# Kernel optimization log

Measured on AMD Instinct MI355X. Metric: run time of the kernel, lower is better.

Reference implementation:

```python
import jax, jax.numpy as jnp
import numpy as np


def setup_inputs() -> dict:
    key = jax.random.key(0)
    ks = jax.random.split(key, 5)
    B, H, W, C = 4, 64, 64, 256
    d = C // 8
    x = jax.random.normal(ks[0], (B, H, W, C), dtype=jnp.float32)
    Wq = jax.random.normal(ks[1], (C, d), dtype=jnp.float32) * (1.0 / np.sqrt(C))
    bq = jnp.zeros((d,), dtype=jnp.float32)
    Wk = jax.random.normal(ks[2], (C, d), dtype=jnp.float32) * (1.0 / np.sqrt(C))
    bk = jnp.zeros((d,), dtype=jnp.float32)
    Wv = jax.random.normal(ks[3], (C, C), dtype=jnp.float32) * (1.0 / np.sqrt(C))
    bv = jnp.zeros((C,), dtype=jnp.float32)
    gamma = jnp.zeros((), dtype=jnp.float32)
    return {"x": x, "Wq": Wq, "bq": bq, "Wk": Wk, "bk": bk, "Wv": Wv, "bv": bv, "gamma": gamma}


def reference(x, Wq, bq, Wk, bk, Wv, bv, gamma):
    B, H, W, C = x.shape
    N = H * W
    xt = x.reshape(B, N, C)  # 1x1 conv == per-pixel dense
    q = xt @ Wq + bq                        # [B, N, d]
    k = xt @ Wk + bk                        # [B, N, d]
    v = xt @ Wv + bv                        # [B, N, C]
    energy = jnp.einsum('bnd,bmd->bnm', q, k)   # Q K^T, [B, N, N]
    attn = jax.nn.softmax(energy, axis=-1)
    # tf: out = matmul(V^T[B,C,N], attn)[B,C,N] then transpose -> out[b,j,c] = sum_i v[b,i,c]*attn[b,i,j]
    out = jnp.einsum('bic,bij->bjc', v, attn)   # [B, N, C]
    out = out.reshape(B, H, W, C)
    return gamma * out + x
```

## Files before the change

kernel.cpp:

```cpp
#include <hip/hip_runtime.h>
#include <hip/hip_bf16.h>


typedef __attribute__((ext_vector_type(4)))  float    f32x4;
typedef __attribute__((ext_vector_type(16))) float    f32x16;
typedef __attribute__((ext_vector_type(8)))  short    bf8;
typedef __attribute__((ext_vector_type(4)))  short    bf4;
typedef __attribute__((ext_vector_type(4)))  unsigned u32x4;

__device__ __forceinline__ short f2bf(float f) {
    unsigned u = __builtin_bit_cast(unsigned, f);
    u += 0x7FFF + ((u >> 16) & 1);
    return (short)(u >> 16);
}
__device__ __forceinline__ float bf2f(short h) {
    unsigned u = ((unsigned)(unsigned short)h) << 16;
    return __builtin_bit_cast(float, u);
}
__device__ __forceinline__ unsigned cvtpk(float lo, float hi) {
    unsigned r;
    asm("v_cvt_pk_bf16_f32 %0, %1, %2" : "=v"(r) : "v"(lo), "v"(hi));
    return r;
}
__device__ __forceinline__ float exp2_fast(float x) {
    float r;
    asm("v_exp_f32 %0, %1" : "=v"(r) : "v"(x));
    return r;
}
__device__ __forceinline__ f32x16 z16() {
    f32x16 v;
#pragma unroll
    for (int i = 0; i < 16; ++i) v[i] = 0.f;
    return v;
}

#define LOG2E 1.44269504088896340736f

__global__ __launch_bounds__(256) void pack_weights(
    const float* __restrict__ Wq, const float* __restrict__ Wk,
    const float* __restrict__ Wv, const float* __restrict__ bq,
    const float* __restrict__ bk, const float* __restrict__ bv,
    short* __restrict__ wallF, float* __restrict__ ball)
{
    int n = blockIdx.x;
    int k = threadIdx.x;
    float w;
    if (n < 32)       w = Wq[k * 32 + n];
    else if (n < 64)  w = Wk[k * 32 + (n - 32)] * LOG2E;
    else              w = Wv[k * 256 + (n - 64)];
    int nf = n >> 4, lcol = n & 15;
    int ks = k >> 5, lg = (k >> 3) & 3, e = k & 7;
    wallF[((size_t)(nf * 8 + ks) * 64 + lg * 16 + lcol) * 8 + e] = f2bf(w);
    if (k == 0) {
        float bias = (n < 32) ? bq[n] : (n < 64) ? bk[n - 32] * LOG2E : bv[n - 64];
        ball[n] = bias;
    }
}

__global__ __launch_bounds__(256) void qkv_gemm(
    const float* __restrict__ x, const short* __restrict__ wallF,
    const float* __restrict__ ball,
    short* __restrict__ qf, short* __restrict__ kf, short* __restrict__ vf)
{
    const int w  = threadIdx.x >> 6;
    const int l  = threadIdx.x & 63;
    const int lr = l & 15;
    const int lg = l >> 4;
    const int m0 = blockIdx.x * 16;

    f32x4 acc[5];
#pragma unroll
    for (int i = 0; i < 5; ++i) acc[i] = (f32x4){0.f, 0.f, 0.f, 0.f};

    const float* xrow = x + (size_t)(m0 + lr) * 256 + lg * 8;
    const short* wwb  = wallF + (size_t)w * 5 * 4096 + l * 8;

#pragma unroll
    for (int ks = 0; ks < 8; ++ks) {
        f32x4 a0 = *(const f32x4*)(xrow + ks * 32);
        f32x4 a1 = *(const f32x4*)(xrow + ks * 32 + 4);
        bf8 af;
#pragma unroll
        for (int t = 0; t < 4; ++t) { af[t] = f2bf(a0[t]); af[t + 4] = f2bf(a1[t]); }
        const short* wb = wwb + (size_t)ks * 512;
#pragma unroll
        for (int nf2 = 0; nf2 < 5; ++nf2) {
            bf8 bfr = *(const bf8*)(wb + (size_t)nf2 * 4096);
            acc[nf2] = __builtin_amdgcn_mfma_f32_16x16x32_bf16(af, bfr, acc[nf2], 0, 0, 0);
        }
    }

    const int b      = m0 >> 12;
    const int i_base = m0 + lg * 4;
#pragma unroll
    for (int nf2 = 0; nf2 < 5; ++nf2) {
        int nf = w * 5 + nf2;
        int n = nf * 16 + lr;
        float bias = ball[n];
        if (nf < 4) {
            int d = n & 31;
            int f = (d >> 4) & 1, sub = (d >> 3) & 1, e = d & 7;
            short* dst = (nf < 2) ? qf : kf;
            size_t base = ((size_t)(b * 128 + (i_base >> 5)) * 2 + f) * 512 + 256 * sub + e;
#pragma unroll
            for (int r = 0; r < 4; ++r) {
                int i31 = (i_base + r) & 31;
                dst[base + (size_t)i31 * 8] = f2bf(acc[nf2][r] + bias);
            }
        } else {
            int c = n - 64;
            bf4 pv;
#pragma unroll
            for (int r = 0; r < 4; ++r) pv[r] = f2bf(acc[nf2][r] + bias);
            size_t addr = (size_t)(b * 256 + (i_base >> 4)) * 4096
                        + (size_t)(c >> 5) * 512
                        + (size_t)((c & 31) + 32 * ((i_base >> 3) & 1)) * 8
                        + (i_base & 7);
            *(bf4*)(vf + addr) = pv;
        }
    }
}

__global__ __launch_bounds__(512) void zsum_kernel(
    const short* __restrict__ qF, const short* __restrict__ kF,
    float* __restrict__ zpart)
{
    const int l = threadIdx.x & 63, w = threadIdx.x >> 6;
    const int b = blockIdx.y;
    const int it0 = blockIdx.x * 2;

    const short* qpa = qF + (size_t)(b * 128 + it0) * 1024 + l * 8;
    bf8 qa0 = *(const bf8*)(qpa);
    bf8 qa1 = *(const bf8*)(qpa + 512);
    bf8 qb0 = *(const bf8*)(qpa + 1024);
    bf8 qb1 = *(const bf8*)(qpa + 1536);

    float zA = 0.f, zB = 0.f;
    const short* kbase = kF + (size_t)b * 131072 + (size_t)w * 16384 + l * 8;
    for (int jt = 0; jt < 16; ++jt) {
        const short* kp = kbase + jt * 1024;
        bf8 kA0 = *(const bf8*)(kp);
        bf8 kA1 = *(const bf8*)(kp + 512);
        f32x16 SA = z16(), SB = z16();
        SA = __builtin_amdgcn_mfma_f32_32x32x16_bf16(kA0, qa0, SA, 0, 0, 0);
        SA = __builtin_amdgcn_mfma_f32_32x32x16_bf16(kA1, qa1, SA, 0, 0, 0);
        SB = __builtin_amdgcn_mfma_f32_32x32x16_bf16(kA0, qb0, SB, 0, 0, 0);
        SB = __builtin_amdgcn_mfma_f32_32x32x16_bf16(kA1, qb1, SB, 0, 0, 0);
#pragma unroll
        for (int r = 0; r < 16; ++r) {
            zA += exp2_fast(fminf(SA[r], 86.f));
            zB += exp2_fast(fminf(SB[r], 86.f));
        }
    }
    zA += __shfl_xor(zA, 32);
    zB += __shfl_xor(zB, 32);
    if (l < 32) {
        zpart[(size_t)w * 16384 + b * 4096 + it0 * 32 + l]      = zA;
        zpart[(size_t)w * 16384 + b * 4096 + it0 * 32 + 32 + l] = zB;
    }
}

__global__ __launch_bounds__(256) void zfinish(
    const float* __restrict__ zpart, float* __restrict__ rz)
{
    int i = blockIdx.x * 256 + threadIdx.x;
    float z = 0.f;
#pragma unroll
    for (int p = 0; p < 8; ++p) z += zpart[p * 16384 + i];
    rz[i] = 1.0f / z;
}

__global__ __launch_bounds__(256) void vscale(
    short* __restrict__ vF, const float* __restrict__ rz)
{
    int t = blockIdx.x * 256 + threadIdx.x;
    size_t base = (size_t)t * 8;
    int b   = (int)(base >> 20);
    int rem = (int)(base & 1048575);
    int it  = rem >> 12;
    int sub = (rem >> 8) & 1;
    int i0  = it * 16 + sub * 8;
    bf8 v = *(bf8*)(vF + base);
    const float* rzp = rz + b * 4096 + i0;
    f32x4 r0 = *(const f32x4*)(rzp);
    f32x4 r1 = *(const f32x4*)(rzp + 4);
#pragma unroll
    for (int e = 0; e < 4; ++e) {
        v[e]     = f2bf(bf2f(v[e])     * r0[e]);
        v[e + 4] = f2bf(bf2f(v[e + 4]) * r1[e]);
    }
    *(bf8*)(vF + base) = v;
}

__global__ __launch_bounds__(512) void attn_out(
    const short* __restrict__ qF, const short* __restrict__ kF,
    const short* __restrict__ vF,
    const float* __restrict__ x, const float* __restrict__ gammaPtr,
    float* __restrict__ out)
{
    __shared__ float red[2][64][128];
    const int l = threadIdx.x & 63, w = threadIdx.x >> 6;
    const int lr = l & 31, hi = l >> 5;
    const int wc = w & 1, isub = w >> 1;

    const int xcd = blockIdx.x & 7, k = blockIdx.x >> 3;
    const int b = xcd >> 1;
    const int jt = (xcd & 1) * 32 + k;
    const int j0 = jt * 64;
    const int c0 = wc * 128;

    bf8 kf0[2], kf1[2];
#pragma unroll
    for (int jf = 0; jf < 2; ++jf) {
        const short* kfp = kF + (size_t)(b * 128 + jt * 2 + jf) * 1024 + l * 8;
        kf0[jf] = *(const bf8*)(kfp);
        kf1[jf] = *(const bf8*)(kfp + 512);
    }

    f32x16 acc[2][4];
#pragma unroll
    for (int jf = 0; jf < 2; ++jf)
#pragma unroll
        for (int cf = 0; cf < 4; ++cf) acc[jf][cf] = z16();

    const short* qbase = qF + (size_t)b * 131072 + l * 8;
    const short* vbase = vF + (size_t)b * 1048576 + (size_t)(c0 >> 5) * 512 + l * 8;

    bf8 q0 = *(const bf8*)(qbase + (size_t)isub * 1024);
    bf8 q1 = *(const bf8*)(qbase + (size_t)isub * 1024 + 512);
    bf8 v0[4];
#pragma unroll
    for (int cf = 0; cf < 4; ++cf)
        v0[cf] = *(const bf8*)(vbase + (size_t)isub * 8192 + cf * 512);

    for (int t = 0; t < 32; ++t) {
        const int m = isub + t * 4;
        const short* vp = vbase + (size_t)m * 8192;
        bf8 cv1[4];
#pragma unroll
        for (int cf = 0; cf < 4; ++cf)
            cv1[cf] = *(const bf8*)(vp + 4096 + cf * 512);
        bf8 nq0 = q0, nq1 = q1, nv0[4];
#pragma unroll
        for (int cf = 0; cf < 4; ++cf) nv0[cf] = v0[cf];
        if (t < 31) {
            const short* qn = qbase + (size_t)(m + 4) * 1024;
            nq0 = *(const bf8*)(qn);
            nq1 = *(const bf8*)(qn + 512);
            const short* vn = vbase + (size_t)(m + 4) * 8192;
#pragma unroll
            for (int cf = 0; cf < 4; ++cf)
                nv0[cf] = *(const bf8*)(vn + cf * 512);
        }

#pragma unroll
        for (int jf = 0; jf < 2; ++jf) {
            f32x16 S = z16();
            S = __builtin_amdgcn_mfma_f32_32x32x16_bf16(q0, kf0[jf], S, 0, 0, 0);
            S = __builtin_amdgcn_mfma_f32_32x32x16_bf16(q1, kf1[jf], S, 0, 0, 0);

            float p[16];
#pragma unroll
            for (int r = 0; r < 16; ++r) p[r] = exp2_fast(fminf(S[r], 86.f));

            unsigned X0 = cvtpk(p[0],  p[1]),  Y0 = cvtpk(p[4],  p[5]);
            unsigned X1 = cvtpk(p[2],  p[3]),  Y1 = cvtpk(p[6],  p[7]);
            unsigned X2 = cvtpk(p[8],  p[9]),  Y2 = cvtpk(p[12], p[13]);
            unsigned X3 = cvtpk(p[10], p[11]), Y3 = cvtpk(p[14], p[15]);
            asm("v_permlane32_swap_b32 %0, %1" : "+v"(X0), "+v"(Y0));
            asm("v_permlane32_swap_b32 %0, %1" : "+v"(X1), "+v"(Y1));
            asm("v_permlane32_swap_b32 %0, %1" : "+v"(X2), "+v"(Y2));
            asm("v_permlane32_swap_b32 %0, %1" : "+v"(X3), "+v"(Y3));
            u32x4 a0w = {X0, X1, Y0, Y1};
            u32x4 a1w = {X2, X3, Y2, Y3};
            bf8 A0 = __builtin_bit_cast(bf8, a0w);
            bf8 A1 = __builtin_bit_cast(bf8, a1w);

            __builtin_amdgcn_s_setprio(1);
#pragma unroll
            for (int cf = 0; cf < 4; ++cf) {
                acc[jf][cf] = __builtin_amdgcn_mfma_f32_32x32x16_bf16(A0, v0[cf],  acc[jf][cf], 0, 0, 0);
                acc[jf][cf] = __builtin_amdgcn_mfma_f32_32x32x16_bf16(A1, cv1[cf], acc[jf][cf], 0, 0, 0);
            }
            __builtin_amdgcn_s_setprio(0);
        }

        q0 = nq0; q1 = nq1;
#pragma unroll
        for (int cf = 0; cf < 4; ++cf) v0[cf] = nv0[cf];
    }

#pragma unroll
    for (int src = 1; src < 4; ++src) {
        if (isub == src) {
#pragma unroll
            for (int jf = 0; jf < 2; ++jf)
#pragma unroll
                for (int cf = 0; cf < 4; ++cf)
#pragma unroll
                    for (int r = 0; r < 16; ++r) {
                        int jrow = (r & 3) + 8 * (r >> 2) + 4 * hi;
                        red[wc][jf * 32 + jrow][cf * 32 + lr] = acc[jf][cf][r];
                    }
        }
        __syncthreads();
        if (isub == 0) {
#pragma unroll
            for (int jf = 0; jf < 2; ++jf)
#pragma unroll
                for (int cf = 0; cf < 4; ++cf)
#pragma unroll
                    for (int r = 0; r < 16; ++r) {
                        int jrow = (r & 3) + 8 * (r >> 2) + 4 * hi;
                        acc[jf][cf][r] += red[wc][jf * 32 + jrow][cf * 32 + lr];
                    }
        }
        __syncthreads();
    }
    if (isub == 0) {
        const float gamma = *gammaPtr;
#pragma unroll
        for (int jf = 0; jf < 2; ++jf)
#pragma unroll
            for (int cf = 0; cf < 4; ++cf)
#pragma unroll
                for (int r = 0; r < 16; ++r) {
                    int jrow = (r & 3) + 8 * (r >> 2) + 4 * hi;
                    int j = j0 + jf * 32 + jrow;
                    size_t idx = (size_t)(b * 4096 + j) * 256 + c0 + cf * 32 + lr;
                    out[idx] = gamma * acc[jf][cf][r] + x[idx];
                }
    }
}

extern "C" void kernel_launch(void* const* d_in, const int* in_sizes, int n_in,
                              void* d_out, int out_size, void* d_ws, size_t ws_size,
                              hipStream_t stream)
{
    const float* x  = (const float*)d_in[0];
    const float* Wq = (const float*)d_in[1];
    const float* bq = (const float*)d_in[2];
    const float* Wk = (const float*)d_in[3];
    const float* bk = (const float*)d_in[4];
    const float* Wv = (const float*)d_in[5];
    const float* bv = (const float*)d_in[6];
    const float* gm = (const float*)d_in[7];
    float* out = (float*)d_out;

    char* wsb = (char*)d_ws;
    short* qf    = (short*)(wsb);
    short* kf    = (short*)(wsb + (1u << 20));
    short* vf    = (short*)(wsb + (2u << 20));
    short* wallF = (short*)(wsb + (10u << 20));
    float* ball  = (float*)(wsb + (10u << 20) + 163840);
    float* zpart = (float*)(wsb + (10u << 20) + 163840 + 1280);
    float* rz    = (float*)(wsb + (10u << 20) + 163840 + 1280 + 524288);

    pack_weights<<<320, 256, 0, stream>>>(Wq, Wk, Wv, bq, bk, bv, wallF, ball);
    qkv_gemm<<<1024, 256, 0, stream>>>(x, wallF, ball, qf, kf, vf);
    zsum_kernel<<<dim3(64, 4), 512, 0, stream>>>(qf, kf, zpart);
    zfinish<<<64, 256, 0, stream>>>(zpart, rz);
    vscale<<<2048, 256, 0, stream>>>(vf, rz);
    attn_out<<<256, 512, 0, stream>>>(qf, kf, vf, x, gm, out);
}
```

Baseline: 98.70 us.

## Split QK^T exp work across wave pairs and share P tiles via LDS

Before this change, the two waves sharing an isub (wc=0/1) each recomputed the same QK^T scores and exp for both j-fragments. Now each wave computes only one j-fragment's probabilities and writes them to a double-buffered LDS buffer. Both waves then read both fragments for the PV MFMAs. The score computation for the next step is software-pipelined one iteration ahead. This halves the redundant exp/MFMA work in the QK stage but adds a __syncthreads per iteration plus LDS writes and reads.

```diff
diff --git a/kernel.cpp b/kernel.cpp
--- a/kernel.cpp
+++ b/kernel.cpp
@@ -198,6 +198,7 @@
     const float* __restrict__ x, const float* __restrict__ gammaPtr,
     float* __restrict__ out)
 {
+    __shared__ short Pb[2][4][2][2][64][8];
     __shared__ float red[2][64][128];
     const int l = threadIdx.x & 63, w = threadIdx.x >> 6;
     const int lr = l & 31, hi = l >> 5;
@@ -209,13 +210,9 @@
     const int j0 = jt * 64;
     const int c0 = wc * 128;
 
-    bf8 kf0[2], kf1[2];
-#pragma unroll
-    for (int jf = 0; jf < 2; ++jf) {
-        const short* kfp = kF + (size_t)(b * 128 + jt * 2 + jf) * 1024 + l * 8;
-        kf0[jf] = *(const bf8*)(kfp);
-        kf1[jf] = *(const bf8*)(kfp + 512);
-    }
+    const short* kfp = kF + (size_t)(b * 128 + jt * 2 + wc) * 1024 + l * 8;
+    bf8 kf0 = *(const bf8*)(kfp);
+    bf8 kf1 = *(const bf8*)(kfp + 512);
 
     f32x16 acc[2][4];
 #pragma unroll
@@ -226,43 +223,68 @@
     const short* qbase = qF + (size_t)b * 131072 + l * 8;
     const short* vbase = vF + (size_t)b * 1048576 + (size_t)(c0 >> 5) * 512 + l * 8;
 
-    bf8 q0 = *(const bf8*)(qbase + (size_t)isub * 1024);
-    bf8 q1 = *(const bf8*)(qbase + (size_t)isub * 1024 + 512);
+    short* myP0 = &Pb[0][isub][wc][0][l][0];
+    short* myP1 = &Pb[0][isub][wc][1][l][0];
+    const size_t PbHalf = sizeof(short) * 4 * 2 * 2 * 64 * 8 / sizeof(short);
+
+    {
+        bf8 q0 = *(const bf8*)(qbase + (size_t)isub * 1024);
+        bf8 q1 = *(const bf8*)(qbase + (size_t)isub * 1024 + 512);
+        f32x16 S = z16();
+        S = __builtin_amdgcn_mfma_f32_32x32x16_bf16(q0, kf0, S, 0, 0, 0);
+        S = __builtin_amdgcn_mfma_f32_32x32x16_bf16(q1, kf1, S, 0, 0, 0);
+        float p[16];
+#pragma unroll
+        for (int r = 0; r < 16; ++r) p[r] = exp2_fast(fminf(S[r], 86.f));
+        unsigned X0 = cvtpk(p[0],  p[1]),  Y0 = cvtpk(p[4],  p[5]);
+        unsigned X1 = cvtpk(p[2],  p[3]),  Y1 = cvtpk(p[6],  p[7]);
+        unsigned X2 = cvtpk(p[8],  p[9]),  Y2 = cvtpk(p[12], p[13]);
+        unsigned X3 = cvtpk(p[10], p[11]), Y3 = cvtpk(p[14], p[15]);
+        asm("v_permlane32_swap_b32 %0, %1" : "+v"(X0), "+v"(Y0));
+        asm("v_permlane32_swap_b32 %0, %1" : "+v"(X1), "+v"(Y1));
+        asm("v_permlane32_swap_b32 %0, %1" : "+v"(X2), "+v"(Y2));
+        asm("v_permlane32_swap_b32 %0, %1" : "+v"(X3), "+v"(Y3));
+        u32x4 a0w = {X0, X1, Y0, Y1};
+        u32x4 a1w = {X2, X3, Y2, Y3};
+        *(bf8*)myP0 = __builtin_bit_cast(bf8, a0w);
+        *(bf8*)myP1 = __builtin_bit_cast(bf8, a1w);
+    }
     bf8 v0[4];
 #pragma unroll
     for (int cf = 0; cf < 4; ++cf)
         v0[cf] = *(const bf8*)(vbase + (size_t)isub * 8192 + cf * 512);
 
     for (int t = 0; t < 32; ++t) {
+        __syncthreads();
         const int m = isub + t * 4;
+        const short* pb = &Pb[t & 1][isub][0][0][l][0];
+        bf8 pa00 = *(const bf8*)(pb);
+        bf8 pa01 = *(const bf8*)(pb + 512);
+        bf8 pa10 = *(const bf8*)(pb + 1024);
+        bf8 pa11 = *(const bf8*)(pb + 1536);
+
         const short* vp = vbase + (size_t)m * 8192;
         bf8 cv1[4];
 #pragma unroll
         for (int cf = 0; cf < 4; ++cf)
             cv1[cf] = *(const bf8*)(vp + 4096 + cf * 512);
-        bf8 nq0 = q0, nq1 = q1, nv0[4];
+        bf8 nv0[4];
 #pragma unroll
         for (int cf = 0; cf < 4; ++cf) nv0[cf] = v0[cf];
         if (t < 31) {
-            const short* qn = qbase + (size_t)(m + 4) * 1024;
-            nq0 = *(const bf8*)(qn);
-            nq1 = *(const bf8*)(qn + 512);
             const short* vn = vbase + (size_t)(m + 4) * 8192;
 #pragma unroll
             for (int cf = 0; cf < 4; ++cf)
                 nv0[cf] = *(const bf8*)(vn + cf * 512);
-        }
-
-#pragma unroll
-        for (int jf = 0; jf < 2; ++jf) {
+            const short* qn = qbase + (size_t)(m + 4) * 1024;
+            bf8 q0 = *(const bf8*)(qn);
+            bf8 q1 = *(const bf8*)(qn + 512);
             f32x16 S = z16();
-            S = __builtin_amdgcn_mfma_f32_32x32x16_bf16(q0, kf0[jf], S, 0, 0, 0);
-            S = __builtin_amdgcn_mfma_f32_32x32x16_bf16(q1, kf1[jf], S, 0, 0, 0);
-
+            S = __builtin_amdgcn_mfma_f32_32x32x16_bf16(q0, kf0, S, 0, 0, 0);
+            S = __builtin_amdgcn_mfma_f32_32x32x16_bf16(q1, kf1, S, 0, 0, 0);
             float p[16];
 #pragma unroll
             for (int r = 0; r < 16; ++r) p[r] = exp2_fast(fminf(S[r], 86.f));
-
             unsigned X0 = cvtpk(p[0],  p[1]),  Y0 = cvtpk(p[4],  p[5]);
             unsigned X1 = cvtpk(p[2],  p[3]),  Y1 = cvtpk(p[6],  p[7]);
             unsigned X2 = cvtpk(p[8],  p[9]),  Y2 = cvtpk(p[12], p[13]);
@@ -273,19 +295,21 @@
             asm("v_permlane32_swap_b32 %0, %1" : "+v"(X3), "+v"(Y3));
             u32x4 a0w = {X0, X1, Y0, Y1};
             u32x4 a1w = {X2, X3, Y2, Y3};
-            bf8 A0 = __builtin_bit_cast(bf8, a0w);
-            bf8 A1 = __builtin_bit_cast(bf8, a1w);
-
-            __builtin_amdgcn_s_setprio(1);
-#pragma unroll
-            for (int cf = 0; cf < 4; ++cf) {
-                acc[jf][cf] = __builtin_amdgcn_mfma_f32_32x32x16_bf16(A0, v0[cf],  acc[jf][cf], 0, 0, 0);
-                acc[jf][cf] = __builtin_amdgcn_mfma_f32_32x32x16_bf16(A1, cv1[cf], acc[jf][cf], 0, 0, 0);
-            }
-            __builtin_amdgcn_s_setprio(0);
-        }
-
-        q0 = nq0; q1 = nq1;
+            short* dst = myP0 + ((t + 1) & 1) * PbHalf;
+            *(bf8*)(dst)       = __builtin_bit_cast(bf8, a0w);
+            *(bf8*)(dst + 512) = __builtin_bit_cast(bf8, a1w);
+        }
+
+        __builtin_amdgcn_s_setprio(1);
+#pragma unroll
+        for (int cf = 0; cf < 4; ++cf) {
+            acc[0][cf] = __builtin_amdgcn_mfma_f32_32x32x16_bf16(pa00, v0[cf],  acc[0][cf], 0, 0, 0);
+            acc[0][cf] = __builtin_amdgcn_mfma_f32_32x32x16_bf16(pa01, cv1[cf], acc[0][cf], 0, 0, 0);
+            acc[1][cf] = __builtin_amdgcn_mfma_f32_32x32x16_bf16(pa10, v0[cf],  acc[1][cf], 0, 0, 0);
+            acc[1][cf] = __builtin_amdgcn_mfma_f32_32x32x16_bf16(pa11, cv1[cf], acc[1][cf], 0, 0, 0);
+        }
+        __builtin_amdgcn_s_setprio(0);
+
 #pragma unroll
         for (int cf = 0; cf < 4; ++cf) v0[cf] = nv0[cf];
     }
```

Result: faster. 94.18 us (-4.6%).
